# Kernel tuning notes

Measured on AMD Instinct MI355X. Metric: run time of the kernel, lower is better.

Reference implementation:

```python
import jax, jax.numpy as jnp
from jax import lax
import numpy as np

B, N, F_IN, T = 8, 2048, 2, 12
K, F_CHEV, F_TIME = 3, 64, 64
LN_EPS = 1e-5


def _cheb_polys(key):
    # random symmetric row-normalized 'scaled Laplacian' proxy, then Chebyshev recurrence
    A = jax.random.uniform(key, (N, N), dtype=jnp.float32)
    A = (A + A.T) * 0.5
    A = A / A.sum(axis=1, keepdims=True)
    L = A - jnp.eye(N, dtype=jnp.float32)  # eigenvalues roughly in [-1, 1]
    Ts = [jnp.eye(N, dtype=jnp.float32), L]
    for _ in range(2, K):
        Ts.append(2.0 * L @ Ts[-1] - Ts[-2])
    return jnp.stack(Ts[:K])  # (K, N, N)


def setup_inputs() -> dict:
    key = jax.random.key(0)
    ks = jax.random.split(key, 20)
    g = lambda i, s: jax.random.normal(ks[i], s, dtype=jnp.float32)
    xav = lambda i, s: g(i, s) * np.sqrt(2.0 / (s[-2] + s[-1]))
    return {
        "x": g(0, (B, N, F_IN, T)),
        "cheb": _cheb_polys(ks[1]),
        "Theta": xav(2, (K, F_IN, F_CHEV)),
        # temporal attention params
        "U1": g(3, (N,)), "U2": xav(4, (F_IN, N)), "U3": g(5, (F_IN,)),
        "be": g(6, (1, T, T)) * 0.1, "Ve": xav(7, (T, T)),
        # spatial attention params
        "W1": g(8, (T,)), "W2": xav(9, (F_IN, T)), "W3": g(10, (F_IN,)),
        "bs": g(11, (1, N, N)) * 0.1, "Vs": xav(12, (N, N)),
        # convs + layernorm
        "tconv_w": g(13, (F_TIME, F_CHEV, 1, 3)) * np.sqrt(2.0 / (F_CHEV * 3 + F_TIME)),
        "tconv_b": jax.random.uniform(ks[14], (F_TIME,), dtype=jnp.float32),
        "rconv_w": g(15, (F_TIME, F_IN, 1, 1)) * np.sqrt(2.0 / (F_IN + F_TIME)),
        "rconv_b": jax.random.uniform(ks[16], (F_TIME,), dtype=jnp.float32),
        "ln_g": jnp.ones((F_TIME,), jnp.float32),
        "ln_b": jnp.zeros((F_TIME,), jnp.float32),
    }


def _forward(x, cheb, Theta, U1, U2, U3, be, Ve, W1, W2, W3, bs, Vs,
             tconv_w, tconv_b, rconv_w, rconv_b, ln_g, ln_b):
    b, n, f, t = x.shape
    # ---- temporal attention: (B,T,T) ----
    lhs_t = jnp.einsum('bnft,n->btf', x, U1) @ U2          # (B,T,N)
    rhs_t = jnp.einsum('f,bnft->bnt', U3, x)               # (B,N,T)
    prod_t = jnp.einsum('btn,bnu->btu', lhs_t, rhs_t)      # (B,T,T)
    E = jnp.einsum('tu,buv->btv', Ve, jax.nn.sigmoid(prod_t + be))
    E = jax.nn.softmax(E, axis=1)
    # apply temporal attention
    x_TAt = (x.reshape(b, n * f, t) @ E).reshape(b, n, f, t)
    # ---- spatial attention: (B,N,N) ----
    lhs_s = jnp.einsum('bnft,t->bnf', x_TAt, W1) @ W2      # (B,N,T)
    rhs_s = jnp.einsum('f,bnft->btn', W3, x_TAt)           # (B,T,N)
    prod_s = jnp.einsum('bnt,btm->bnm', lhs_s, rhs_s)      # (B,N,N)
    S = jnp.einsum('mn,bnp->bmp', Vs, jax.nn.sigmoid(prod_s + bs))
    S = jax.nn.softmax(S, axis=1)
    # ---- Chebyshev graph conv with spatial attention (vectorized over k, t) ----
    # rhs[b,k,n,f,t] = sum_m (cheb[k,m,n] * S[b,m,n]) * x[b,m,f,t]
    rhs = jnp.einsum('kmn,bmn,bmft->bknft', cheb, S, x)
    gcn = jax.nn.relu(jnp.einsum('bknft,kfo->bnot', rhs, Theta))  # (B,N,F_chev,T)
    # ---- time conv (1x3, pad 1 along T) + 1x1 residual conv ----
    dn = ('NCHW', 'OIHW', 'NCHW')
    tc = lax.conv_general_dilated(gcn.transpose(0, 2, 1, 3), tconv_w, (1, 1),
                                  ((0, 0), (1, 1)), dimension_numbers=dn)
    tc = tc + tconv_b[None, :, None, None]                 # (B,F_time,N,T)
    res = lax.conv_general_dilated(x.transpose(0, 2, 1, 3), rconv_w, (1, 1),
                                   ((0, 0), (0, 0)), dimension_numbers=dn)
    res = res + rconv_b[None, :, None, None]
    y = jax.nn.relu(res + tc).transpose(0, 3, 2, 1)        # (B,T,N,F_time)
    mu = y.mean(-1, keepdims=True)
    var = jnp.mean((y - mu) ** 2, axis=-1, keepdims=True)
    y = (y - mu) * lax.rsqrt(var + LN_EPS) * ln_g + ln_b
    return y.transpose(0, 2, 3, 1)                          # (B,N,F_time,T)


def reference(x, cheb, Theta, U1, U2, U3, be, Ve, W1, W2, W3, bs, Vs,
              tconv_w, tconv_b, rconv_w, rconv_b, ln_g, ln_b):
    return _forward(x, cheb, Theta, U1, U2, U3, be, Ve, W1, W2, W3, bs, Vs,
                    tconv_w, tconv_b, rconv_w, rconv_b, ln_g, ln_b)
```

## Files before the change

kernel.cpp:

```cpp
#include <hip/hip_runtime.h>
#include <cstdint>
#include <cstddef>

#define NB 8
#define NN 2048
#define MCV 16

using bf16x8 = __attribute__((ext_vector_type(8))) __bf16;
using f32x4  = __attribute__((ext_vector_type(4))) float;

__device__ __forceinline__ float bf2f(unsigned short u) {
  union { unsigned int i; float f; } v; v.i = ((unsigned int)u) << 16; return v.f;
}
__device__ __forceinline__ unsigned short f2bf(float f) {
  union { float f; unsigned int i; } v; v.f = f;
  unsigned int lsb = (v.i >> 16) & 1u;
  v.i += 0x7fffu + lsb;
  return (unsigned short)(v.i >> 16);
}
__device__ __forceinline__ float ld_in(const void* p, size_t idx, int mode) {
  return mode ? bf2f(((const unsigned short*)p)[idx]) : ((const float*)p)[idx];
}
__device__ __forceinline__ int get_mode(const void* chebp) {
  return ((const unsigned int*)chebp)[0] != 0x3F800000u;
}

#define GLOAD16(gptr, lptr) \
  __builtin_amdgcn_global_load_lds((const __attribute__((address_space(1))) void*)(gptr), \
                                   (__attribute__((address_space(3))) void*)(lptr), 16, 0, 0)

struct Seg { const void* src; void* dst; int count; int tobf; };
struct ConvArgs { Seg s[16]; };

__global__ void k_convert(ConvArgs a, const void* __restrict__ chebp) {
  const int mode = get_mode(chebp);
  const int stride = gridDim.x * blockDim.x;
  for (int si = 0; si < 16; ++si) {
    const Seg sg = a.s[si];
    for (int i = blockIdx.x * blockDim.x + threadIdx.x; i < sg.count; i += stride) {
      float v = ld_in(sg.src, i, mode);
      if (sg.tobf) ((unsigned short*)sg.dst)[i] = f2bf(v);
      else         ((float*)sg.dst)[i] = v;
    }
  }
}

__global__ void k_vsb(const void* __restrict__ vs, unsigned short* __restrict__ out,
                      const void* __restrict__ tw, unsigned short* __restrict__ twr,
                      const void* __restrict__ chebp) {
  const int mode = get_mode(chebp);
  const int idx = blockIdx.x * 256 + threadIdx.x;
  if (idx < NN * NN) {
    const int ke = idx & 7, row = (idx >> 3) & 127, kc = (idx >> 10) & 7;
    const int hf = (idx >> 13) & 1, kt = (idx >> 14) & 31, mt = idx >> 19;
    const int m = mt * 256 + hf * 128 + row, k = kt * 64 + kc * 8 + ke;
    out[idx] = f2bf(ld_in(vs, (size_t)m * NN + k, mode));
  } else {
    const int j = idx - NN * NN;
    if (j < 12288) {
      const int dt = j >> 12, rem = j & 4095, o = rem >> 6, c = rem & 63;
      twr[j] = f2bf(ld_in(tw, (size_t)o * 192 + c * 3 + dt, mode));
    }
  }
}

__global__ __launch_bounds__(256) void k_temp1(const float* __restrict__ xf,
      const float* __restrict__ U1f, const float* __restrict__ U2f, const float* __restrict__ U3f,
      const float* __restrict__ bef, const float* __restrict__ Vef, float* __restrict__ E) {
  const int b = blockIdx.x;
  float accL[24], accG[24];
#pragma unroll
  for (int i = 0; i < 24; i++) { accL[i] = 0.f; accG[i] = 0.f; }
  const float u30 = U3f[0], u31 = U3f[1];
  for (int n = threadIdx.x; n < NN; n += 256) {
    const float* xp = xf + ((size_t)b * NN + n) * 24;
    const float u1 = U1f[n], u20 = U2f[n], u21 = U2f[NN + n];
#pragma unroll
    for (int t = 0; t < 12; t++) {
      float x0 = xp[t], x1 = xp[12 + t];
      accL[t * 2 + 0] += u1 * x0;
      accL[t * 2 + 1] += u1 * x1;
      float xs = u30 * x0 + u31 * x1;
      accG[t]      += u20 * xs;
      accG[12 + t] += u21 * xs;
    }
  }
#pragma unroll
  for (int i = 0; i < 24; i++) {
#pragma unroll
    for (int d = 32; d >= 1; d >>= 1) {
      accL[i] += __shfl_xor(accL[i], d, 64);
      accG[i] += __shfl_xor(accG[i], d, 64);
    }
  }
  __shared__ float red[4][48];
  __shared__ float L[48];
  __shared__ float s0[12][12], e1[12][12];
  const int lane = threadIdx.x & 63, wv = threadIdx.x >> 6;
  if (lane == 0) {
#pragma unroll
    for (int i = 0; i < 24; i++) { red[wv][i] = accL[i]; red[wv][24 + i] = accG[i]; }
  }
  __syncthreads();
  if (threadIdx.x < 48)
    L[threadIdx.x] = red[0][threadIdx.x] + red[1][threadIdx.x]
                   + red[2][threadIdx.x] + red[3][threadIdx.x];
  __syncthreads();
  const int tid = threadIdx.x;
  const int t = tid / 12, v = tid % 12;
  if (tid < 144) {
    float pr = L[t * 2 + 0] * L[24 + v] + L[t * 2 + 1] * L[36 + v] + bef[t * 12 + v];
    s0[t][v] = 1.f / (1.f + __expf(-pr));
  }
  __syncthreads();
  if (tid < 144) {
    float s = 0.f;
#pragma unroll
    for (int u = 0; u < 12; u++) s += Vef[t * 12 + u] * s0[u][v];
    e1[t][v] = s;
  }
  __syncthreads();
  if (tid < 144) {
    float mx = -1e30f;
#pragma unroll
    for (int u = 0; u < 12; u++) mx = fmaxf(mx, e1[u][v]);
    float sm = 0.f;
#pragma unroll
    for (int u = 0; u < 12; u++) sm += __expf(e1[u][v] - mx);
    E[b * 144 + t * 12 + v] = __expf(e1[t][v] - mx) / sm;
  }
}

__global__ __launch_bounds__(256) void k_xtat(const float* __restrict__ xf,
      const float* __restrict__ E, const float* __restrict__ W1f, const float* __restrict__ W2f,
      const float* __restrict__ W3f, float* __restrict__ lhs, float* __restrict__ rhsS) {
  const int b = blockIdx.y;
  const int n = blockIdx.x * 256 + threadIdx.x;
  __shared__ float Es[144];
  if (threadIdx.x < 144) Es[threadIdx.x] = E[b * 144 + threadIdx.x];
  __syncthreads();
  const float* xp = xf + ((size_t)b * NN + n) * 24;
  float xv[24];
#pragma unroll
  for (int i = 0; i < 24; i++) xv[i] = xp[i];
  float xT[24];
#pragma unroll
  for (int f = 0; f < 2; f++)
#pragma unroll
    for (int v = 0; v < 12; v++) {
      float s = 0.f;
#pragma unroll
      for (int u = 0; u < 12; u++) s += xv[f * 12 + u] * Es[u * 12 + v];
      xT[f * 12 + v] = s;
    }
  float a0 = 0.f, a1 = 0.f;
#pragma unroll
  for (int v = 0; v < 12; v++) { a0 += xT[v] * W1f[v]; a1 += xT[12 + v] * W1f[v]; }
  const float w30 = W3f[0], w31 = W3f[1];
  float* lp = lhs + ((size_t)b * NN + n) * 12;
#pragma unroll
  for (int t = 0; t < 12; t++) {
    lp[t] = a0 * W2f[t] + a1 * W2f[12 + t];
    rhsS[((size_t)b * 12 + t) * NN + n] = w30 * xT[t] + w31 * xT[12 + t];
  }
}

__global__ __launch_bounds__(256) void k_sig(const float* __restrict__ lhs,
      const float* __restrict__ rhsS, const void* __restrict__ bs,
      unsigned short* __restrict__ sigT, const void* __restrict__ chebp, int p0, int PL) {
  const int tid = threadIdx.x;
  const int n = blockIdx.x * 256 + tid;
  const int pg0 = p0 + blockIdx.y * 16;
  const int mode = get_mode(chebp);
  __shared__ float rsl[8][12][16];
  for (int i = tid; i < 1536; i += 256) {
    int b = i / 192, t = (i % 192) / 16, c = i % 16;
    rsl[b][t][c] = rhsS[((size_t)b * 12 + t) * NN + pg0 + c];
  }
  float bsv[16];
  if (mode) {
    const int4* bp = (const int4*)((const unsigned short*)bs + (size_t)n * NN + pg0);
    int4 q0 = bp[0], q1 = bp[1];
    const unsigned short* u0 = (const unsigned short*)&q0;
    const unsigned short* u1 = (const unsigned short*)&q1;
#pragma unroll
    for (int i = 0; i < 8; i++) { bsv[i] = bf2f(u0[i]); bsv[8 + i] = bf2f(u1[i]); }
  } else {
    const float4* fp = (const float4*)((const float*)bs + (size_t)n * NN + pg0);
#pragma unroll
    for (int q = 0; q < 4; q++) {
      float4 v = fp[q];
      bsv[q * 4 + 0] = v.x; bsv[q * 4 + 1] = v.y; bsv[q * 4 + 2] = v.z; bsv[q * 4 + 3] = v.w;
    }
  }
  __syncthreads();
  const size_t kpart = (size_t)(n >> 6) * 16384 + (size_t)((n >> 3) & 7) * 1024 + (n & 7);
  const int plbase = pg0 - p0;
  for (int b = 0; b < 8; b++) {
    float lv[12];
    const float* lp = lhs + ((size_t)b * NN + n) * 12;
#pragma unroll
    for (int t = 0; t < 12; t++) lv[t] = lp[t];
    const int gbase = b * PL + plbase;
    const size_t gt_off = (size_t)(gbase >> 8) * 524288 + (size_t)((gbase >> 7) & 1) * 8192
                        + (size_t)(gbase & 127) * 8;
#pragma unroll
    for (int pp = 0; pp < 16; pp++) {
      float acc = bsv[pp];
#pragma unroll
      for (int t = 0; t < 12; t++) acc += lv[t] * rsl[b][t][pp];
      float sg = 1.f / (1.f + __expf(-acc));
      sigT[gt_off + (size_t)pp * 8 + kpart] = f2bf(sg);
    }
  }
}

__global__ __launch_bounds__(512, 2) void k_gemm(const unsigned short* __restrict__ A,
      const unsigned short* __restrict__ Bm, unsigned short* __restrict__ C,
      float* __restrict__ pmax, float* __restrict__ psum,
      int PL, int plshift, int GP, int nwg) {
  __shared__ __align__(16) unsigned short lA[2][16384];
  __shared__ __align__(16) unsigned short lB[2][16384];
  const int id = blockIdx.x;
  const int cpx = nwg >> 3;
  const int sid = (id & 7) * cpx + (id >> 3);
  const int s = sid >> 4, w = sid & 15;
  const int mt = (s & 1) * 4 + (w & 3);
  const int pt = (s >> 1) * 4 + (w >> 2);
  const int tid = threadIdx.x;
  const int wv = tid >> 6, lane = tid & 63;
  const int fr = lane & 15, hi = lane >> 4;
  const int wr = wv >> 2, wc = wv & 3;
  const unsigned short* gA = A  + (size_t)mt * 524288;
  const unsigned short* gB = Bm + (size_t)pt * 524288;

  f32x4 acc[8][4] = {};
  bf16x8 af[8][2], bfr[4][2];

#define STAGE_H(h) do { \
    const int kt_ = (h) >> 2, part_ = (h) & 3, r_ = part_ & 1; \
    const unsigned short* gsrc_ = ((part_ < 2) ? gA : gB) + (size_t)kt_ * 16384 + r_ * 8192 + tid * 8; \
    unsigned short* ldst_ = ((part_ < 2) ? &lA[0][0] : &lB[0][0]) + (kt_ & 1) * 16384 + r_ * 8192 + wv * 512; \
    GLOAD16(gsrc_,        ldst_); \
    GLOAD16(gsrc_ + 4096, ldst_ + 4096); \
  } while (0)

#define READ_A03(bf) do { \
    _Pragma("unroll") for (int mi_ = 0; mi_ < 4; ++mi_) \
    _Pragma("unroll") for (int s2_ = 0; s2_ < 2; ++s2_) \
      af[mi_][s2_] = *(const bf16x8*)&lA[bf][wr * 8192 + (s2_ * 4 + hi) * 1024 + (mi_ * 16 + fr) * 8]; \
  } while (0)

#define READ_A47(bf) do { \
    _Pragma("unroll") for (int mi_ = 4; mi_ < 8; ++mi_) \
    _Pragma("unroll") for (int s2_ = 0; s2_ < 2; ++s2_) \
      af[mi_][s2_] = *(const bf16x8*)&lA[bf][wr * 8192 + (s2_ * 4 + hi) * 1024 + (mi_ * 16 + fr) * 8]; \
  } while (0)

#define READ_B01(bf) do { \
    _Pragma("unroll") for (int ni_ = 0; ni_ < 2; ++ni_) \
    _Pragma("unroll") for (int s2_ = 0; s2_ < 2; ++s2_) \
      bfr[ni_][s2_] = *(const bf16x8*)&lB[bf][(wc >> 1) * 8192 + (s2_ * 4 + hi) * 1024 \
                                             + ((wc & 1) * 64 + ni_ * 16 + fr) * 8]; \
  } while (0)

#define READ_B23(bf) do { \
    _Pragma("unroll") for (int ni_ = 2; ni_ < 4; ++ni_) \
    _Pragma("unroll") for (int s2_ = 0; s2_ < 2; ++s2_) \
      bfr[ni_][s2_] = *(const bf16x8*)&lB[bf][(wc >> 1) * 8192 + (s2_ * 4 + hi) * 1024 \
                                             + ((wc & 1) * 64 + ni_ * 16 + fr) * 8]; \
  } while (0)

#define MFMA_Q(mh, nh) do { \
    __builtin_amdgcn_s_setprio(1); \
    _Pragma("unroll") for (int s2_ = 0; s2_ < 2; ++s2_) \
    _Pragma("unroll") for (int mi_ = 0; mi_ < 4; ++mi_) \
    _Pragma("unroll") for (int ni_ = 0; ni_ < 2; ++ni_) \
      acc[(mh) * 4 + mi_][(nh) * 2 + ni_] = __builtin_amdgcn_mfma_f32_16x16x32_bf16( \
          af[(mh) * 4 + mi_][s2_], bfr[(nh) * 2 + ni_][s2_], acc[(mh) * 4 + mi_][(nh) * 2 + ni_], 0, 0, 0); \
    __builtin_amdgcn_s_setprio(0); \
  } while (0)

#define PH_BAR() __builtin_amdgcn_s_barrier()
#define PH_LGKM() asm volatile("s_waitcnt lgkmcnt(0)" ::: "memory")

  for (int h = 0; h < 8; ++h) STAGE_H(h);
  asm volatile("s_waitcnt vmcnt(8)" ::: "memory");
  PH_BAR();

#pragma unroll 1
  for (int i = 0; i < 16; ++i) {
    const int hb = 8 * i;
    const bool more = (i < 15);
    READ_A03(0); READ_B01(0);
    if (i > 0) STAGE_H(hb + 4);
    PH_BAR(); PH_LGKM();
    MFMA_Q(0, 0);
    PH_BAR();
    READ_B23(0);
    if (i > 0) STAGE_H(hb + 5);
    PH_BAR(); PH_LGKM();
    MFMA_Q(0, 1);
    PH_BAR();
    READ_A47(0);
    if (more) STAGE_H(hb + 10);
    PH_BAR(); PH_LGKM();
    MFMA_Q(1, 0);
    PH_BAR();
    if (more) STAGE_H(hb + 11);
    PH_BAR(); PH_LGKM();
    MFMA_Q(1, 1);
    if (more || i == 0) asm volatile("s_waitcnt vmcnt(4)" ::: "memory");
    else                asm volatile("s_waitcnt vmcnt(0)" ::: "memory");
    PH_BAR();
    READ_A03(1); READ_B01(1);
    if (more) STAGE_H(hb + 8);
    PH_BAR(); PH_LGKM();
    MFMA_Q(0, 0);
    PH_BAR();
    READ_B23(1);
    if (more) STAGE_H(hb + 9);
    PH_BAR(); PH_LGKM();
    MFMA_Q(0, 1);
    PH_BAR();
    READ_A47(1);
    if (more) STAGE_H(hb + 14);
    PH_BAR(); PH_LGKM();
    MFMA_Q(1, 0);
    PH_BAR();
    if (more) STAGE_H(hb + 15);
    PH_BAR(); PH_LGKM();
    MFMA_Q(1, 1);
    if (more) asm volatile("s_waitcnt vmcnt(4)" ::: "memory");
    else      asm volatile("s_waitcnt vmcnt(0)" ::: "memory");
    PH_BAR();
  }
#undef STAGE_H
#undef READ_A03
#undef READ_A47
#undef READ_B01
#undef READ_B23
#undef MFMA_Q
#undef PH_BAR
#undef PH_LGKM

  const int m0 = mt * 256, gcol0 = pt * 256;
  const int plmask = PL - 1;
#pragma unroll
  for (int ni = 0; ni < 4; ++ni) {
    float lmax = -1e30f;
    float vr[8][4];
#pragma unroll
    for (int mi = 0; mi < 8; ++mi) {
      const int g = gcol0 + wc * 64 + ni * 16 + fr;
      const int b = g >> plshift, pl = g & plmask;
      const int mrow = m0 + wr * 128 + mi * 16 + hi * 4;
      unsigned short* cp = C + ((size_t)b * NN + mrow) * PL + pl;
#pragma unroll
      for (int r = 0; r < 4; r++) {
        unsigned short us = f2bf(acc[mi][ni][r]);
        cp[(size_t)r * PL] = us;
        vr[mi][r] = bf2f(us);
        lmax = fmaxf(lmax, vr[mi][r]);
      }
    }
    float lsum = 0.f;
#pragma unroll
    for (int mi = 0; mi < 8; ++mi)
#pragma unroll
      for (int r = 0; r < 4; r++) lsum += __expf(vr[mi][r] - lmax);
#pragma unroll
    for (int d = 16; d <= 32; d <<= 1) {
      float omax = __shfl_xor(lmax, d, 64);
      float osum = __shfl_xor(lsum, d, 64);
      float nm = fmaxf(lmax, omax);
      lsum = lsum * __expf(lmax - nm) + osum * __expf(omax - nm);
      lmax = nm;
    }
    if (hi == 0) {
      const int part = mt * 2 + wr;
      const int g = gcol0 + wc * 64 + ni * 16 + lane;
      pmax[(size_t)part * GP + g] = lmax;
      psum[(size_t)part * GP + g] = lsum;
    }
  }
}

__global__ __launch_bounds__(256) void k_cheb(const unsigned short* __restrict__ S0c,
        const void* __restrict__ cheb, const unsigned short* __restrict__ cbf, int use_cbf,
        const float* __restrict__ xf, const float* __restrict__ pmax, const float* __restrict__ psum,
        unsigned short* __restrict__ part, int p0, int PL, int mspan, int GP) {
  const int b = blockIdx.z, mc = blockIdx.y;
  const int pl = blockIdx.x * 256 + threadIdx.x;
  const int n = p0 + pl;
  const int mode = get_mode(cheb);
  const int g = b * PL + pl;
  float mx = -1e30f;
#pragma unroll
  for (int c = 0; c < 16; c++) mx = fmaxf(mx, pmax[(size_t)c * GP + g]);
  float sm = 0.f;
#pragma unroll
  for (int c = 0; c < 16; c++) sm += psum[(size_t)c * GP + g] * __expf(pmax[(size_t)c * GP + g] - mx);
  const float inv = 1.f / sm;
  float acc[3][24];
#pragma unroll
  for (int k = 0; k < 3; k++)
#pragma unroll
    for (int j = 0; j < 24; j++) acc[k][j] = 0.f;
  const unsigned short* s0p = S0c + (size_t)b * NN * PL + pl;
  const int mEnd = mc * mspan + mspan;
  if (use_cbf || mode) {
    const unsigned short* cb = (use_cbf ? cbf : (const unsigned short*)cheb) + n;
#pragma unroll 2
    for (int m = mc * mspan; m < mEnd; ++m) {
      float w = __expf(bf2f(s0p[(size_t)m * PL]) - mx) * inv;
      const f32x4* xp = (const f32x4*)(xf + ((size_t)b * NN + m) * 24);
      float w0 = w * bf2f(cb[(size_t)m * NN]);
      float w1 = w * bf2f(cb[(size_t)NN * NN + (size_t)m * NN]);
      float w2 = w * bf2f(cb[(size_t)2 * NN * NN + (size_t)m * NN]);
#pragma unroll
      for (int q = 0; q < 6; q++) {
        f32x4 xv = xp[q];
#pragma unroll
        for (int e = 0; e < 4; e++) {
          int j = q * 4 + e;
          acc[0][j] += w0 * xv[e];
          acc[1][j] += w1 * xv[e];
          acc[2][j] += w2 * xv[e];
        }
      }
    }
  } else {
    const float* cb = (const float*)cheb + n;
#pragma unroll 2
    for (int m = mc * mspan; m < mEnd; ++m) {
      float w = __expf(bf2f(s0p[(size_t)m * PL]) - mx) * inv;
      const f32x4* xp = (const f32x4*)(xf + ((size_t)b * NN + m) * 24);
      float w0 = w * cb[(size_t)m * NN];
      float w1 = w * cb[(size_t)NN * NN + (size_t)m * NN];
      float w2 = w * cb[(size_t)2 * NN * NN + (size_t)m * NN];
#pragma unroll
      for (int q = 0; q < 6; q++) {
        f32x4 xv = xp[q];
#pragma unroll
        for (int e = 0; e < 4; e++) {
          int j = q * 4 + e;
          acc[0][j] += w0 * xv[e];
          acc[1][j] += w1 * xv[e];
          acc[2][j] += w2 * xv[e];
        }
      }
    }
  }
  unsigned short* pp = part + ((size_t)(mc * 8 + b) * 72) * PL + pl;
#pragma unroll
  for (int k = 0; k < 3; k++)
#pragma unroll
    for (int j = 0; j < 24; j++) pp[(size_t)(k * 24 + j) * PL] = f2bf(acc[k][j]);
}

__global__ void k_chebred(const unsigned short* __restrict__ part, float* __restrict__ rhsC,
                          int p0, int PL) {
  const int idx = blockIdx.x * 256 + threadIdx.x;
  if (idx >= 8 * 72 * PL) return;
  const int pl = idx % PL;
  const int r = idx / PL;
  const int j = r % 72, b = r / 72;
  float s = 0.f;
  for (int mc = 0; mc < MCV; ++mc)
    s += bf2f(part[((size_t)(mc * 8 + b) * 72 + j) * PL + pl]);
  rhsC[((size_t)b * NN + p0 + pl) * 72 + j] = s;
}

__global__ __launch_bounds__(256) void k_final(const float* __restrict__ rhsC,
      const float* __restrict__ Thf, const unsigned short* __restrict__ twr,
      const float* __restrict__ tbf, const float* __restrict__ rwf, const float* __restrict__ rbf,
      const float* __restrict__ lngf, const float* __restrict__ lnbf,
      const float* __restrict__ xf, void* __restrict__ out, const void* __restrict__ chebp) {
  const int mode = get_mode(chebp);
  __shared__ __align__(16) unsigned short ltw[192 * 72];
  __shared__ __align__(16) unsigned short gT[4][18][72];
  __shared__ float rl[4][72];
  __shared__ float prm[6][64];
  const int tid = threadIdx.x;
  const int wv = tid >> 6, lane = tid & 63;
  const size_t bn = (size_t)blockIdx.x * 4 + wv;

  for (int i = tid; i < 1536; i += 256) {
    const int row = i >> 3, cseg = (i & 7) * 8;
    *(bf16x8*)&ltw[row * 72 + cseg] = *(const bf16x8*)&twr[row * 64 + cseg];
  }
  if (tid < 64) {
    prm[0][tid] = tbf[tid] + rbf[tid];
    prm[1][tid] = rwf[tid * 2];
    prm[2][tid] = rwf[tid * 2 + 1];
    prm[3][tid] = lngf[tid];
    prm[4][tid] = lnbf[tid];
  }
  for (int i = lane; i < 648; i += 64) ((unsigned int*)&gT[wv][0][0])[i] = 0u;
  {
    const float* rp = rhsC + bn * 72;
    rl[wv][lane] = rp[lane];
    if (lane < 8) rl[wv][64 + lane] = rp[64 + lane];
  }
  __syncthreads();
  {
    const int c = lane;
    float th[6];
#pragma unroll
    for (int kf = 0; kf < 6; kf++) th[kf] = Thf[kf * 64 + c];
#pragma unroll
    for (int t = 0; t < 12; t++) {
      float s = 0.f;
#pragma unroll
      for (int kf = 0; kf < 6; kf++) s += rl[wv][kf * 12 + t] * th[kf];
      gT[wv][1 + t][c] = f2bf(fmaxf(s, 0.f));
    }
  }
  __syncthreads();
  const int fr = lane & 15, hi = lane >> 4;
  f32x4 acc4[4] = {};
#pragma unroll
  for (int dt = 0; dt < 3; dt++)
#pragma unroll
    for (int ks = 0; ks < 2; ks++) {
      bf16x8 bfrag = *(const bf16x8*)&gT[wv][fr + dt][ks * 32 + hi * 8];
#pragma unroll
      for (int ot = 0; ot < 4; ot++) {
        bf16x8 afrag = *(const bf16x8*)&ltw[(dt * 64 + ot * 16 + fr) * 72 + ks * 32 + hi * 8];
        acc4[ot] = __builtin_amdgcn_mfma_f32_16x16x32_bf16(afrag, bfrag, acc4[ot], 0, 0, 0);
      }
    }
  const int t = fr;
  const int tc = t < 12 ? t : 11;
  const float x0 = xf[bn * 24 + tc], x1 = xf[bn * 24 + 12 + tc];
  float vals[4][4];
  float sum = 0.f, sumsq = 0.f;
#pragma unroll
  for (int ot = 0; ot < 4; ot++) {
    f32x4 rbt4 = *(const f32x4*)&prm[0][ot * 16 + hi * 4];
    f32x4 rw04 = *(const f32x4*)&prm[1][ot * 16 + hi * 4];
    f32x4 rw14 = *(const f32x4*)&prm[2][ot * 16 + hi * 4];
#pragma unroll
    for (int r = 0; r < 4; r++) {
      float v = acc4[ot][r] + rbt4[r] + rw04[r] * x0 + rw14[r] * x1;
      v = fmaxf(v, 0.f);
      vals[ot][r] = v;
      sum += v; sumsq += v * v;
    }
  }
  sum   += __shfl_xor(sum, 16, 64);
  sumsq += __shfl_xor(sumsq, 16, 64);
  sum   += __shfl_xor(sum, 32, 64);
  sumsq += __shfl_xor(sumsq, 32, 64);
  const float mu = sum * (1.f / 64.f);
  const float var = sumsq * (1.f / 64.f) - mu * mu;
  const float rs = rsqrtf(var + 1e-5f);
  if (t < 12) {
#pragma unroll
    for (int ot = 0; ot < 4; ot++) {
      f32x4 lg4 = *(const f32x4*)&prm[3][ot * 16 + hi * 4];
      f32x4 lb4 = *(const f32x4*)&prm[4][ot * 16 + hi * 4];
#pragma unroll
      for (int r = 0; r < 4; r++) {
        const int o = ot * 16 + hi * 4 + r;
        float y = (vals[ot][r] - mu) * rs * lg4[r] + lb4[r];
        if (mode) ((unsigned short*)out)[bn * 768 + o * 12 + t] = f2bf(y);
        else      ((float*)out)[bn * 768 + o * 12 + t] = y;
      }
    }
  }
}

struct Plan {
  size_t o_xf, o_Th, o_U1, o_U2, o_U3, o_be, o_Ve, o_W1, o_W2, o_W3,
         o_twr, o_tb, o_rw, o_rb, o_lg, o_lb, o_Vs,
         o_E, o_lhs, o_rhsS, o_rhsC,
         o_R1, o_S0, o_pmax, o_psum, o_cbf;
  size_t total;
};

static Plan make_plan(int PL, int cbf) {
  Plan p; size_t off = 0;
  auto al = [&](size_t b) { size_t r = off; off += (b + 255) & ~(size_t)255; return r; };
  const int GP = 8 * PL;
  p.o_xf   = al((size_t)NB * NN * 24 * 4);
  p.o_Th   = al(384 * 4);
  p.o_U1   = al(2048 * 4);
  p.o_U2   = al(4096 * 4);
  p.o_U3   = al(2 * 4);
  p.o_be   = al(144 * 4);
  p.o_Ve   = al(144 * 4);
  p.o_W1   = al(12 * 4);
  p.o_W2   = al(24 * 4);
  p.o_W3   = al(2 * 4);
  p.o_twr  = al(12288 * 2);
  p.o_tb   = al(64 * 4);
  p.o_rw   = al(128 * 4);
  p.o_rb   = al(64 * 4);
  p.o_lg   = al(64 * 4);
  p.o_lb   = al(64 * 4);
  p.o_Vs   = al((size_t)NN * NN * 2);
  p.o_E    = al(NB * 144 * 4);
  p.o_lhs  = al((size_t)NB * NN * 12 * 4);
  p.o_rhsS = al((size_t)NB * 12 * NN * 4);
  p.o_rhsC = al((size_t)NB * NN * 72 * 4);
  p.o_R1   = al((size_t)32768 * PL);
  p.o_S0   = al((size_t)NB * NN * PL * 2);
  p.o_pmax = al((size_t)16 * GP * 4);
  p.o_psum = al((size_t)16 * GP * 4);
  p.o_cbf  = cbf ? al((size_t)3 * NN * NN * 2) : 0;
  p.total = off;
  return p;
}

extern "C" void kernel_launch(void* const* d_in, const int* in_sizes, int n_in,
                              void* d_out, int out_size, void* d_ws, size_t ws_size,
                              hipStream_t stream) {
  (void)in_sizes; (void)n_in; (void)out_size;
  char* ws = (char*)d_ws;

  int PL, use_cbf;
  if      (make_plan(1024, 1).total <= ws_size) { PL = 1024; use_cbf = 1; }
  else if (make_plan(1024, 0).total <= ws_size) { PL = 1024; use_cbf = 0; }
  else if (make_plan(512, 1).total  <= ws_size) { PL = 512;  use_cbf = 1; }
  else                                          { PL = 512;  use_cbf = 0; }
  const Plan P = make_plan(PL, use_cbf);
  const int GP = 8 * PL;
  const int plshift = (PL == 512) ? 9 : 10;
  const int mspan = NN / MCV;
  const void* chebp = d_in[1];

  float* xf   = (float*)(ws + P.o_xf);
  float* Ebuf = (float*)(ws + P.o_E);
  float* lhs  = (float*)(ws + P.o_lhs);
  float* rhsS = (float*)(ws + P.o_rhsS);
  float* rhsC = (float*)(ws + P.o_rhsC);
  unsigned short* sigT = (unsigned short*)(ws + P.o_R1);
  unsigned short* part = (unsigned short*)(ws + P.o_R1);
  unsigned short* S0c  = (unsigned short*)(ws + P.o_S0);
  float* pmax = (float*)(ws + P.o_pmax);
  float* psum = (float*)(ws + P.o_psum);
  unsigned short* cbfp = use_cbf ? (unsigned short*)(ws + P.o_cbf)
                                 : (unsigned short*)d_in[1];

  ConvArgs ca;
  auto seg = [&](int i, int di, size_t o, int count, int tobf) {
    ca.s[i].src = d_in[di]; ca.s[i].dst = (void*)(ws + o); ca.s[i].count = count; ca.s[i].tobf = tobf;
  };
  seg(0, 0, P.o_xf, 393216, 0);
  seg(1, 2, P.o_Th, 384, 0);
  seg(2, 3, P.o_U1, 2048, 0);
  seg(3, 4, P.o_U2, 4096, 0);
  seg(4, 5, P.o_U3, 2, 0);
  seg(5, 6, P.o_be, 144, 0);
  seg(6, 7, P.o_Ve, 144, 0);
  seg(7, 8, P.o_W1, 12, 0);
  seg(8, 9, P.o_W2, 24, 0);
  seg(9, 10, P.o_W3, 2, 0);
  seg(10, 14, P.o_tb, 64, 0);
  seg(11, 15, P.o_rw, 128, 0);
  seg(12, 16, P.o_rb, 64, 0);
  seg(13, 17, P.o_lg, 64, 0);
  seg(14, 18, P.o_lb, 64, 0);
  seg(15, 1, P.o_cbf, use_cbf ? 3 * NN * NN : 0, 1);
  k_convert<<<1024, 256, 0, stream>>>(ca, chebp);
  k_vsb<<<(NN * NN + 12288 + 255) / 256, 256, 0, stream>>>(d_in[12],
      (unsigned short*)(ws + P.o_Vs), d_in[13], (unsigned short*)(ws + P.o_twr), chebp);

  k_temp1<<<NB, 256, 0, stream>>>(xf, (float*)(ws + P.o_U1), (float*)(ws + P.o_U2),
                                  (float*)(ws + P.o_U3), (float*)(ws + P.o_be),
                                  (float*)(ws + P.o_Ve), Ebuf);
  k_xtat<<<dim3(8, NB), 256, 0, stream>>>(xf, Ebuf, (float*)(ws + P.o_W1), (float*)(ws + P.o_W2),
                                          (float*)(ws + P.o_W3), lhs, rhsS);

  const int nwg = 8 * (GP / 256);
  for (int p0 = 0; p0 < NN; p0 += PL) {
    k_sig<<<dim3(8, PL / 16), 256, 0, stream>>>(lhs, rhsS, d_in[11], sigT, chebp, p0, PL);
    k_gemm<<<nwg, 512, 0, stream>>>((unsigned short*)(ws + P.o_Vs), sigT, S0c,
                                    pmax, psum, PL, plshift, GP, nwg);
    k_cheb<<<dim3(PL / 256, MCV, NB), 256, 0, stream>>>(S0c, d_in[1], cbfp, use_cbf,
                                                        xf, pmax, psum, part, p0, PL, mspan, GP);
    k_chebred<<<(8 * 72 * PL + 255) / 256, 256, 0, stream>>>(part, rhsC, p0, PL);
  }

  k_final<<<NB * NN / 4, 256, 0, stream>>>(rhsC, (float*)(ws + P.o_Th),
      (unsigned short*)(ws + P.o_twr), (float*)(ws + P.o_tb), (float*)(ws + P.o_rw),
      (float*)(ws + P.o_rb), (float*)(ws + P.o_lg), (float*)(ws + P.o_lb), xf, d_out, chebp);
}
```

Before: 361.4 us.

## Stage sigmoid tiles in LDS for vector stores, trim GEMM barriers, reorder epilogue

In k_sig, each thread now writes its bf16 sigmoid values into a shared tile, and the block then writes them to the swizzled sigT layout as 16-byte vector stores instead of scattered 2-byte stores. This adds two block barriers per batch iteration. In k_gemm, the barrier before each lgkmcnt wait is removed, and in two phases that have no new LDS reads the wait is dropped entirely. This cuts synchronisation but risks LDS read/write hazards with the staging writes. The GEMM epilogue also computes the softmax partials first and stores C afterwards in a separate loop, changing the order of the global stores.

```diff
diff --git a/kernel.cpp b/kernel.cpp
--- a/kernel.cpp
+++ b/kernel.cpp
@@ -169,10 +169,12 @@
       const float* __restrict__ rhsS, const void* __restrict__ bs,
       unsigned short* __restrict__ sigT, const void* __restrict__ chebp, int p0, int PL) {
   const int tid = threadIdx.x;
-  const int n = blockIdx.x * 256 + tid;
+  const int n0 = blockIdx.x * 256;
+  const int n = n0 + tid;
   const int pg0 = p0 + blockIdx.y * 16;
   const int mode = get_mode(chebp);
   __shared__ float rsl[8][12][16];
+  __shared__ __align__(16) unsigned short sh[16][264];
   for (int i = tid; i < 1536; i += 256) {
     int b = i / 192, t = (i % 192) / 16, c = i % 16;
     rsl[b][t][c] = rhsS[((size_t)b * 12 + t) * NN + pg0 + c];
@@ -194,24 +196,31 @@
     }
   }
   __syncthreads();
-  const size_t kpart = (size_t)(n >> 6) * 16384 + (size_t)((n >> 3) & 7) * 1024 + (n & 7);
   const int plbase = pg0 - p0;
+  const size_t nbase = (size_t)(n0 >> 6) * 16384;
   for (int b = 0; b < 8; b++) {
     float lv[12];
     const float* lp = lhs + ((size_t)b * NN + n) * 12;
 #pragma unroll
     for (int t = 0; t < 12; t++) lv[t] = lp[t];
+#pragma unroll
+    for (int pp = 0; pp < 16; pp++) {
+      float acc = bsv[pp];
+#pragma unroll
+      for (int t = 0; t < 12; t++) acc += lv[t] * rsl[b][t][pp];
+      float sg = 1.f / (1.f + __expf(-acc));
+      sh[pp][tid] = f2bf(sg);
+    }
+    __syncthreads();
     const int gbase = b * PL + plbase;
     const size_t gt_off = (size_t)(gbase >> 8) * 524288 + (size_t)((gbase >> 7) & 1) * 8192
-                        + (size_t)(gbase & 127) * 8;
-#pragma unroll
-    for (int pp = 0; pp < 16; pp++) {
-      float acc = bsv[pp];
-#pragma unroll
-      for (int t = 0; t < 12; t++) acc += lv[t] * rsl[b][t][pp];
-      float sg = 1.f / (1.f + __expf(-acc));
-      sigT[gt_off + (size_t)pp * 8 + kpart] = f2bf(sg);
-    }
+                        + (size_t)(gbase & 127) * 8 + nbase;
+    for (int c = tid; c < 512; c += 256) {
+      const int growL = c & 15, k3 = (c >> 4) & 7, n6 = c >> 7;
+      int4 v = *(const int4*)&sh[growL][n6 * 64 + k3 * 8];
+      *(int4*)&sigT[gt_off + (size_t)growL * 8 + (size_t)k3 * 1024 + (size_t)n6 * 16384] = v;
+    }
+    __syncthreads();
   }
 }
 
@@ -294,42 +303,40 @@
     const bool more = (i < 15);
     READ_A03(0); READ_B01(0);
     if (i > 0) STAGE_H(hb + 4);
-    PH_BAR(); PH_LGKM();
+    PH_LGKM();
     MFMA_Q(0, 0);
     PH_BAR();
     READ_B23(0);
     if (i > 0) STAGE_H(hb + 5);
-    PH_BAR(); PH_LGKM();
+    PH_LGKM();
     MFMA_Q(0, 1);
     PH_BAR();
     READ_A47(0);
     if (more) STAGE_H(hb + 10);
-    PH_BAR(); PH_LGKM();
+    PH_LGKM();
     MFMA_Q(1, 0);
     PH_BAR();
     if (more) STAGE_H(hb + 11);
-    PH_BAR(); PH_LGKM();
     MFMA_Q(1, 1);
-    if (more || i == 0) asm volatile("s_waitcnt vmcnt(4)" ::: "memory");
-    else                asm volatile("s_waitcnt vmcnt(0)" ::: "memory");
+    if (more) asm volatile("s_waitcnt vmcnt(4)" ::: "memory");
+    else      asm volatile("s_waitcnt vmcnt(0)" ::: "memory");
     PH_BAR();
     READ_A03(1); READ_B01(1);
     if (more) STAGE_H(hb + 8);
-    PH_BAR(); PH_LGKM();
+    PH_LGKM();
     MFMA_Q(0, 0);
     PH_BAR();
     READ_B23(1);
     if (more) STAGE_H(hb + 9);
-    PH_BAR(); PH_LGKM();
+    PH_LGKM();
     MFMA_Q(0, 1);
     PH_BAR();
     READ_A47(1);
     if (more) STAGE_H(hb + 14);
-    PH_BAR(); PH_LGKM();
+    PH_LGKM();
     MFMA_Q(1, 0);
     PH_BAR();
     if (more) STAGE_H(hb + 15);
-    PH_BAR(); PH_LGKM();
     MFMA_Q(1, 1);
     if (more) asm volatile("s_waitcnt vmcnt(4)" ::: "memory");
     else      asm volatile("s_waitcnt vmcnt(0)" ::: "memory");
@@ -349,26 +356,20 @@
 #pragma unroll
   for (int ni = 0; ni < 4; ++ni) {
     float lmax = -1e30f;
-    float vr[8][4];
-#pragma unroll
-    for (int mi = 0; mi < 8; ++mi) {
-      const int g = gcol0 + wc * 64 + ni * 16 + fr;
-      const int b = g >> plshift, pl = g & plmask;
-      const int mrow = m0 + wr * 128 + mi * 16 + hi * 4;
-      unsigned short* cp = C + ((size_t)b * NN + mrow) * PL + pl;
+    float vv[8][4];
+#pragma unroll
+    for (int mi = 0; mi < 8; ++mi)
 #pragma unroll
       for (int r = 0; r < 4; r++) {
-        unsigned short us = f2bf(acc[mi][ni][r]);
-        cp[(size_t)r * PL] = us;
-        vr[mi][r] = bf2f(us);
-        lmax = fmaxf(lmax, vr[mi][r]);
+        float x = bf2f(f2bf(acc[mi][ni][r]));
+        vv[mi][r] = x;
+        lmax = fmaxf(lmax, x);
       }
-    }
     float lsum = 0.f;
 #pragma unroll
     for (int mi = 0; mi < 8; ++mi)
 #pragma unroll
-      for (int r = 0; r < 4; r++) lsum += __expf(vr[mi][r] - lmax);
+      for (int r = 0; r < 4; r++) lsum += __expf(vv[mi][r] - lmax);
 #pragma unroll
     for (int d = 16; d <= 32; d <<= 1) {
       float omax = __shfl_xor(lmax, d, 64);
@@ -382,6 +383,19 @@
       const int g = gcol0 + wc * 64 + ni * 16 + lane;
       pmax[(size_t)part * GP + g] = lmax;
       psum[(size_t)part * GP + g] = lsum;
+    }
+  }
+#pragma unroll
+  for (int mi = 0; mi < 8; ++mi) {
+#pragma unroll
+    for (int r = 0; r < 4; r++) {
+      const int mrow = m0 + wr * 128 + mi * 16 + hi * 4 + r;
+#pragma unroll
+      for (int ni = 0; ni < 4; ++ni) {
+        const int g = gcol0 + wc * 64 + ni * 16 + fr;
+        const int b = g >> plshift, pl = g & plmask;
+        C[((size_t)b * NN + mrow) * PL + pl] = f2bf(acc[mi][ni][r]);
+      }
     }
   }
 }
```

Result: faster. 349.8 us (-3.2%).
